# Kernel tuning notes

Measured on AMD Instinct MI355X. Metric: run time of the kernel, lower is better.

The kernel has to match this reference:

```python
import jax, jax.numpy as jnp
import numpy as np

THRESHOLD = 0.5
NEG_POS_RATIO = 3
ALPHA = 10.0


def cxcy_to_xy(c):
    return jnp.concatenate([c[..., :2] - c[..., 2:] / 2, c[..., :2] + c[..., 2:] / 2], axis=-1)


def xy_to_cxcy(xy):
    return jnp.concatenate([(xy[..., :2] + xy[..., 2:]) / 2, xy[..., 2:] - xy[..., :2]], axis=-1)


def encode(cxcy, anc):
    # SSD encoding with variances 0.1 / 0.2 expressed as /10 and *5
    return jnp.concatenate([
        (cxcy[..., :2] - anc[..., :2]) / (anc[..., 2:] / 10.0),
        jnp.log(cxcy[..., 2:] / anc[..., 2:]) * 5.0,
    ], axis=-1)


def jaccard(a, b):
    # a: [N,4] corner boxes, b: [P,4] corner boxes -> [N,P] IoU
    lt = jnp.maximum(a[:, None, :2], b[None, :, :2])
    rb = jnp.minimum(a[:, None, 2:], b[None, :, 2:])
    wh = jnp.clip(rb - lt, 0.0)
    inter = wh[..., 0] * wh[..., 1]
    area_a = (a[:, 2] - a[:, 0]) * (a[:, 3] - a[:, 1])
    area_b = (b[:, 2] - b[:, 0]) * (b[:, 3] - b[:, 1])
    return inter / (area_a[:, None] + area_b[None, :] - inter)


def _match(boxes, labels, corner_anchor, center_anchor):
    # boxes: [N_obj,4] corner, labels: [N_obj]
    n_obj = boxes.shape[0]
    iou = jaccard(boxes, corner_anchor)                 # [N_obj, P]
    obj_idx = jnp.argmax(iou, axis=1)                   # best prior per object
    iou = iou.at[jnp.arange(n_obj), obj_idx].set(1.0)   # force-match best prior
    positive = jnp.any(iou >= THRESHOLD, axis=0)        # [P]
    max_prior_idx = jnp.argmax(iou, axis=0)             # best object per prior
    true_cls = (labels[max_prior_idx] + 1) * positive.astype(jnp.int32)
    true_locs = encode(xy_to_cxcy(boxes[max_prior_idx]), center_anchor)
    return positive, true_cls, true_locs


def setup_inputs() -> dict:
    B, P, C, NOBJ = 32, 24564, 21, 24
    keys = jax.random.split(jax.random.key(0), 7)
    pred_cls = jax.random.normal(keys[0], (B, P, C), dtype=jnp.float32)
    pred_loc = jax.random.normal(keys[1], (B, P, 4), dtype=jnp.float32) * 0.1
    cxy = jax.random.uniform(keys[2], (B, NOBJ, 2), minval=0.2, maxval=0.8)
    wh = jax.random.uniform(keys[3], (B, NOBJ, 2), minval=0.05, maxval=0.3)
    gt_boxes = jnp.clip(jnp.concatenate([cxy - wh / 2, cxy + wh / 2], axis=-1), 0.0, 1.0)
    gt_labels = jax.random.randint(keys[4], (B, NOBJ), 0, C - 1, dtype=jnp.int32)
    a_cxy = jax.random.uniform(keys[5], (P, 2), minval=0.0, maxval=1.0)
    a_wh = jax.random.uniform(keys[6], (P, 2), minval=0.05, maxval=0.4)
    center_anchor = jnp.concatenate([a_cxy, a_wh], axis=-1)
    return {"pred_cls": pred_cls, "pred_loc": pred_loc, "gt_boxes": gt_boxes,
            "gt_labels": gt_labels, "center_anchor": center_anchor}


def reference(pred_cls, pred_loc, gt_boxes, gt_labels, center_anchor):
    B, P, C = pred_cls.shape
    corner_anchor = cxcy_to_xy(center_anchor)
    positive, true_cls, true_locs = jax.vmap(_match, in_axes=(0, 0, None, None))(
        gt_boxes, gt_labels, corner_anchor, center_anchor)

    n_pos = positive.sum(axis=1)                        # [B]
    n_pos_total = n_pos.sum().astype(pred_loc.dtype)

    # localization: L1 mean over positive priors (4 coords each)
    pos_f = positive[..., None].astype(pred_loc.dtype)
    loc_loss = (jnp.abs(pred_loc - true_locs) * pos_f).sum() / (n_pos_total * 4.0)

    # per-element cross entropy [B, P]
    logp = jax.nn.log_softmax(pred_cls, axis=-1)
    ce = -jnp.take_along_axis(logp, true_cls[..., None], axis=-1)[..., 0]

    conf_pos = (ce * positive.astype(ce.dtype)).sum()
    ce_neg = jnp.where(positive, 0.0, ce)
    ce_neg_sorted = jnp.sort(ce_neg, axis=1)[:, ::-1]   # descending
    ranks = jnp.arange(P)[None, :]
    hard_mask = (ranks < (NEG_POS_RATIO * n_pos)[:, None]).astype(ce.dtype)
    conf_neg = (ce_neg_sorted * hard_mask).sum()
    conf_loss = (conf_pos + conf_neg) / n_pos_total

    loc_loss = ALPHA * loc_loss
    total_loss = conf_loss + loc_loss
    return total_loss, (conf_loss, loc_loss)
```

## Files before the change

kernel.cpp:

```cpp
#include <hip/hip_runtime.h>
#include <stdint.h>

#define B 32
#define P 24564
#define NCLS 21
#define NOBJ 24
#define THRESH 0.5f
#define NBKT 2048
#define LCAP 6144
#define BKT_BASE 7232

#define OFF_ACC      0
#define OFF_ARRV     24
#define OFF_NPOS     32
#define HDR_WORDS    40
#define OFF_OBJPART  160
#define OFF_HIST     98464
#define OFF_CENEG    360608

typedef unsigned long long u64;
__device__ __forceinline__ u64 umax64(u64 a, u64 b) { return a > b ? a : b; }

__device__ __forceinline__ int ce_bucket(unsigned bits) {
    int bk = (int)(bits >> 17) - BKT_BASE;
    return bk < 0 ? 0 : (bk > 2047 ? 2047 : bk);
}

__global__ __launch_bounds__(256) void k_objmax(
    const float* __restrict__ gt_boxes, const float* __restrict__ anchor,
    char* __restrict__ ws) {
#pragma clang fp contract(off)
    int b = blockIdx.y;
    int j = blockIdx.x;
    int tid = threadIdx.x;
    unsigned* hist = (unsigned*)(ws + OFF_HIST);
    u64* part = (u64*)(ws + OFF_OBJPART);
    if (tid < 128) hist[(b * 16 + j) * 128 + tid] = 0u;
    if (b == 0 && j == 0 && tid < HDR_WORDS) ((unsigned*)ws)[tid] = 0u;
    __shared__ float4 sbox[NOBJ];
    __shared__ u64 sbest[NOBJ];
    if (tid < NOBJ) {
        const float* g = gt_boxes + (size_t)(b * NOBJ + tid) * 4;
        sbox[tid] = make_float4(g[0], g[1], g[2], g[3]);
        sbest[tid] = 0ull;
    }
    __syncthreads();
    u64 best[NOBJ];
#pragma unroll
    for (int n = 0; n < NOBJ; n++) best[n] = 0ull;
    int pend = min(P, (j + 1) * 1536);
    for (int p = j * 1536 + tid; p < pend; p += 256) {
        float4 a = *(const float4*)(anchor + (size_t)p * 4);
        float ax0 = a.x - a.z * 0.5f, ay0 = a.y - a.w * 0.5f;
        float ax1 = a.x + a.z * 0.5f, ay1 = a.y + a.w * 0.5f;
        float area_a = (ax1 - ax0) * (ay1 - ay0);
        unsigned pk = ~(unsigned)p;
#pragma unroll
        for (int n = 0; n < NOBJ; n++) {
            float4 bx = sbox[n];
            float ltx = fmaxf(bx.x, ax0), lty = fmaxf(bx.y, ay0);
            float rbx = fminf(bx.z, ax1), rby = fminf(bx.w, ay1);
            float w = fmaxf(rbx - ltx, 0.f), h = fmaxf(rby - lty, 0.f);
            float inter = w * h;
            float area_o = (bx.z - bx.x) * (bx.w - bx.y);
            float iou = inter / (area_o + area_a - inter);
            u64 key = ((u64)__float_as_uint(iou) << 32) | pk;
            best[n] = umax64(best[n], key);
        }
    }
#pragma unroll
    for (int n = 0; n < NOBJ; n++) {
        u64 v = best[n];
        for (int off = 32; off > 0; off >>= 1) v = umax64(v, __shfl_down(v, off, 64));
        if ((tid & 63) == 0) atomicMax(&sbest[n], v);
    }
    __syncthreads();
    if (tid < NOBJ) part[((size_t)b * NOBJ + tid) * 16 + j] = sbest[tid];
}

__global__ __launch_bounds__(256, 4) void k_mainB(
    const float* __restrict__ pred_cls, const float* __restrict__ pred_loc,
    const float* __restrict__ gt_boxes, const int* __restrict__ gt_labels,
    const float* __restrict__ anchor, char* __restrict__ ws) {
    double* acc = (double*)(ws + OFF_ACC);
    int* n_pos = (int*)(ws + OFF_NPOS);
    const u64* objpart = (const u64*)(ws + OFF_OBJPART);
    unsigned* hist = (unsigned*)(ws + OFF_HIST);
    float* ce_neg = (float*)(ws + OFF_CENEG);

    __shared__ float4 sbox[NOBJ];
    __shared__ float sarea[NOBJ];
    __shared__ int slab[NOBJ];
    __shared__ int sobj[NOBJ];
    __shared__ unsigned shist[NBKT];
    __shared__ float swf[8];
    __shared__ int swi[4];
    const int tid = threadIdx.x;
    const int b = blockIdx.x / 48;
    const int j = blockIdx.x % 48;

    for (int i = tid; i < NBKT; i += 256) shist[i] = 0u;
    if (tid < NOBJ) {
        const float* g = gt_boxes + (size_t)(b * NOBJ + tid) * 4;
        sbox[tid] = make_float4(g[0], g[1], g[2], g[3]);
        sarea[tid] = (g[2] - g[0]) * (g[3] - g[1]);
        slab[tid] = gt_labels[b * NOBJ + tid];
        const u64* pp = objpart + ((size_t)b * NOBJ + tid) * 16;
        u64 m = pp[0];
#pragma unroll
        for (int q = 1; q < 16; q++) m = umax64(m, pp[q]);
        sobj[tid] = (int)(~(unsigned)(m & 0xFFFFFFFFull));
    }
    __syncthreads();

    int p0 = j * 512 + tid * 2;
    float lsum = 0.f, cpos = 0.f;
    int lnp = 0;
    if (p0 < P) {
        float2 xx[21];
        const float2* xp = (const float2*)(pred_cls + ((size_t)b * P + p0) * NCLS);
#pragma unroll
        for (int k = 0; k < 21; k++) xx[k] = xp[k];
        const float* arr = (const float*)xx;
        float4 anc2[2];
        anc2[0] = ((const float4*)anchor)[p0];
        anc2[1] = ((const float4*)anchor)[p0 + 1];
        float2 cev;
        float* cevp = (float*)&cev;
#pragma unroll
        for (int r = 0; r < 2; r++) {
            int p = p0 + r;
            float4 a = anc2[r];
            float ax0 = a.x - a.z * 0.5f, ay0 = a.y - a.w * 0.5f;
            float ax1 = a.x + a.z * 0.5f, ay1 = a.y + a.w * 0.5f;
            float area_a = (ax1 - ax0) * (ay1 - ay0);
            float bv = -1.f;
            int bn = 0;
#pragma unroll
            for (int n = 0; n < NOBJ; n++) {
                float4 bx = sbox[n];
                float ltx = fmaxf(bx.x, ax0), lty = fmaxf(bx.y, ay0);
                float rbx = fminf(bx.z, ax1), rby = fminf(bx.w, ay1);
                float w = fmaxf(rbx - ltx, 0.f), h = fmaxf(rby - lty, 0.f);
                float inter = w * h;
                float den = sarea[n] + area_a - inter;
                float iou = inter * __builtin_amdgcn_rcpf(den);
                if (p == sobj[n]) iou = 1.0f;
                if (iou > bv) { bv = iou; bn = n; }
            }
            int pos = (bv >= THRESH) ? 1 : 0;
            int cls = pos ? (slab[bn] + 1) : 0;
            const float* x = arr + r * 21;
            float m = x[0];
#pragma unroll
            for (int q = 1; q < NCLS; q++) m = fmaxf(m, x[q]);
            float s = 0.f;
#pragma unroll
            for (int q = 0; q < NCLS; q++) s += __expf(x[q] - m);
            float xc = x[0];
#pragma unroll
            for (int q = 1; q < NCLS; q++) xc = (cls == q) ? x[q] : xc;
            float ce = m + __logf(s) - xc;
            if (pos) {
                lnp++;
                cpos += ce;
                cevp[r] = 0.f;
                float4 bx = sbox[bn];
                float bcx = (bx.x + bx.z) * 0.5f, bcy = (bx.y + bx.w) * 0.5f;
                float bw = bx.z - bx.x, bh = bx.w - bx.y;
                float t0 = (bcx - a.x) / (a.z / 10.0f);
                float t1 = (bcy - a.y) / (a.w / 10.0f);
                float t2 = __logf(bw / a.z) * 5.0f;
                float t3 = __logf(bh / a.w) * 5.0f;
                float4 pl = *(const float4*)(pred_loc + ((size_t)b * P + p) * 4);
                lsum += fabsf(pl.x - t0) + fabsf(pl.y - t1) + fabsf(pl.z - t2) + fabsf(pl.w - t3);
            } else {
                float cen = fmaxf(ce, 0.f);
                cevp[r] = cen;
                atomicAdd(&shist[ce_bucket(__float_as_uint(cen))], 1u);
            }
        }
        *(float2*)(ce_neg + (size_t)b * P + p0) = cev;
    }
    for (int off = 32; off > 0; off >>= 1) {
        lsum += __shfl_down(lsum, off, 64);
        cpos += __shfl_down(cpos, off, 64);
        lnp  += __shfl_down(lnp, off, 64);
    }
    if ((tid & 63) == 0) { swf[tid >> 6] = lsum; swf[4 + (tid >> 6)] = cpos; swi[tid >> 6] = lnp; }
    __syncthreads();
    if (tid == 0) {
        float ls = swf[0] + swf[1] + swf[2] + swf[3];
        float cs = swf[4] + swf[5] + swf[6] + swf[7];
        int np = swi[0] + swi[1] + swi[2] + swi[3];
        if (np) atomicAdd(&n_pos[b], np);
        atomicAdd(&acc[0], (double)ls);
        atomicAdd(&acc[1], (double)cs);
    }
    for (int i = tid; i < NBKT; i += 256) {
        unsigned c = shist[i];
        if (c) atomicAdd(&hist[b * NBKT + i], c);
    }
}

__device__ __forceinline__ void find_bound(const unsigned* shist, int NB, int K,
                                           int* sscal, unsigned* wsum, int tid) {
    int G = NB >> 8;
    unsigned loc[8];
    unsigned tot = 0, v = 0;
    if (tid < 256) {
        for (int g = 0; g < G; g++) { loc[g] = shist[tid * G + g]; tot += loc[g]; }
        v = tot;
        int lane = tid & 63;
        for (int off = 1; off < 64; off <<= 1) {
            unsigned o = __shfl_down(v, off, 64);
            if (lane + off < 64) v += o;
        }
        if (lane == 0) wsum[tid >> 6] = v;
    }
    __syncthreads();
    if (tid < 256) {
        unsigned above = 0;
        for (int w = (tid >> 6) + 1; w < 4; w++) above += wsum[w];
        unsigned sfx_excl = above + (v - tot);
        unsigned snext = 0, sloc = 0;
        for (int k = G - 1; k >= 0; k--) {
            sloc = snext + loc[k];
            unsigned sfx_i = sloc + sfx_excl;
            unsigned sfx_n = snext + sfx_excl;
            if (sfx_i >= (unsigned)K && sfx_n < (unsigned)K) {
                sscal[0] = tid * G + k;
                sscal[1] = K - (int)sfx_n;
            }
            snext = sloc;
        }
        if (tid == 0) {
            unsigned total = sloc + sfx_excl;
            if (total < (unsigned)K) {
                sscal[0] = 0;
                sscal[1] = K - (int)((sloc - loc[0]) + sfx_excl);
            }
        }
    }
    __syncthreads();
}

__device__ __forceinline__ void find_bound64(const unsigned* h64, int K, int* sscal, int tid) {
    if (tid < 64) {
        unsigned cnt = h64[tid];
        unsigned v = cnt;
        for (int off = 1; off < 64; off <<= 1) {
            unsigned o = __shfl_down(v, off, 64);
            if (tid + off < 64) v += o;
        }
        unsigned vnext = v - cnt;
        if (v >= (unsigned)K && vnext < (unsigned)K) { sscal[0] = tid; sscal[1] = K - (int)vnext; }
    }
    __syncthreads();
}

__device__ __forceinline__ int bsum16i(int v, int* buf, int tid) {
    for (int off = 32; off > 0; off >>= 1) v += __shfl_down(v, off, 64);
    if ((tid & 63) == 0) buf[tid >> 6] = v;
    __syncthreads();
    int r = 0;
#pragma unroll
    for (int w = 0; w < 16; w++) r += buf[w];
    __syncthreads();
    return r;
}

__global__ __launch_bounds__(1024) void k_sel(
    const float* __restrict__ ce_neg, const unsigned* __restrict__ hist,
    const int* __restrict__ n_pos, double* __restrict__ acc,
    unsigned* __restrict__ arrv, float* __restrict__ out) {
    __shared__ unsigned shist[NBKT];
    __shared__ unsigned slist[LCAP];
    __shared__ int swi[16];
    __shared__ double swd[16];
    __shared__ unsigned wsum[4];
    __shared__ int sscal[4];
    const int b = blockIdx.x;
    const int tid = threadIdx.x;
    int K = n_pos[b] * 3;
    if (K > P) K = P;
    double s = 0.0;
    if (K > 0) {
        for (int i = tid; i < NBKT; i += 1024) shist[i] = hist[b * NBKT + i];
        __syncthreads();
        find_bound(shist, NBKT, K, sscal, wsum, tid);
        int b0 = sscal[0], Kp0 = sscal[1];
        if (tid == 0) sscal[2] = 0;
        __syncthreads();
        const uint4* x4 = (const uint4*)(ce_neg + (size_t)b * P);
        for (int i = tid; i < P / 4; i += 1024) {
            uint4 v = x4[i];
            unsigned vv[4] = {v.x, v.y, v.z, v.w};
#pragma unroll
            for (int r = 0; r < 4; r++) {
                int bk = ce_bucket(vv[r]);
                if (bk > b0) s += (double)__uint_as_float(vv[r]);
                else if (bk == b0) {
                    int pos = atomicAdd(&sscal[2], 1);
                    if (pos < LCAP) slist[pos] = vv[r];
                }
            }
        }
        __syncthreads();
        int lcnt = sscal[2];
        if (Kp0 > 0) {
            bool clamped = (b0 == 0) || (b0 == 2047);
            if (lcnt <= LCAP && !clamped) {
                for (int i = tid; i < NBKT; i += 1024) shist[i] = 0u;
                __syncthreads();
                for (int i = tid; i < lcnt; i += 1024)
                    atomicAdd(&shist[(slist[i] >> 6) & 0x7FFu], 1u);
                __syncthreads();
                find_bound(shist, NBKT, Kp0, sscal, wsum, tid);
                int b1 = sscal[0], Kp1 = sscal[1];
                if (tid < 64) shist[tid] = 0u;
                __syncthreads();
                for (int i = tid; i < lcnt; i += 1024) {
                    unsigned v = slist[i];
                    int k1 = (int)((v >> 6) & 0x7FFu);
                    if (k1 > b1) s += (double)__uint_as_float(v);
                    else if (k1 == b1) atomicAdd(&shist[v & 0x3Fu], 1u);
                }
                __syncthreads();
                find_bound64(shist, Kp1, sscal, tid);
                int b2 = sscal[0], R = sscal[1];
                for (int i = tid; i < lcnt; i += 1024) {
                    unsigned v = slist[i];
                    if ((int)((v >> 6) & 0x7FFu) == b1 && (int)(v & 0x3Fu) > b2)
                        s += (double)__uint_as_float(v);
                }
                unsigned Tbits = ((unsigned)(b0 + BKT_BASE) << 17) | ((unsigned)b1 << 6) | (unsigned)b2;
                if (tid == 0) s += (double)R * (double)__uint_as_float(Tbits);
            } else if (lcnt <= LCAP) {
                unsigned T = 0;
                for (int bit = 30; bit >= 0; bit--) {
                    unsigned cand = T | (1u << bit);
                    int cc = 0;
                    for (int i = tid; i < lcnt; i += 1024) cc += (slist[i] >= cand) ? 1 : 0;
                    int tot = bsum16i(cc, swi, tid);
                    if (tot >= Kp0) T = cand;
                }
                int cgt = 0;
                for (int i = tid; i < lcnt; i += 1024) {
                    unsigned v = slist[i];
                    if (v > T) { cgt++; s += (double)__uint_as_float(v); }
                }
                int cg = bsum16i(cgt, swi, tid);
                if (tid == 0) s += (double)(Kp0 - cg) * (double)__uint_as_float(T);
            } else {
                const unsigned* src = (const unsigned*)(ce_neg + (size_t)b * P);
                unsigned T = 0;
                for (int bit = 30; bit >= 0; bit--) {
                    unsigned cand = T | (1u << bit);
                    int cc = 0;
                    for (int i = tid; i < P; i += 1024) {
                        unsigned v = src[i];
                        if (ce_bucket(v) == b0 && v >= cand) cc++;
                    }
                    int tot = bsum16i(cc, swi, tid);
                    if (tot >= Kp0) T = cand;
                }
                int cgt = 0;
                for (int i = tid; i < P; i += 1024) {
                    unsigned v = src[i];
                    if (ce_bucket(v) == b0 && v > T) { cgt++; s += (double)__uint_as_float(v); }
                }
                int cg = bsum16i(cgt, swi, tid);
                if (tid == 0) s += (double)(Kp0 - cg) * (double)__uint_as_float(T);
            }
        }
        for (int off = 32; off > 0; off >>= 1) s += __shfl_down(s, off, 64);
        if ((tid & 63) == 0) swd[tid >> 6] = s;
        __syncthreads();
        if (tid == 0) {
            double tot = 0.0;
#pragma unroll
            for (int w = 0; w < 16; w++) tot += swd[w];
            atomicAdd(&acc[2], tot);
        }
    }
    __syncthreads();
    if (tid == 0) {
        __threadfence();
        unsigned done = __hip_atomic_fetch_add(arrv, 1u, __ATOMIC_ACQ_REL,
                                               __HIP_MEMORY_SCOPE_AGENT);
        if (done == B - 1) {
            int npt = 0;
            for (int k = 0; k < B; k++)
                npt += __hip_atomic_load((int*)&n_pos[k], __ATOMIC_RELAXED,
                                         __HIP_MEMORY_SCOPE_AGENT);
            u64 u0 = __hip_atomic_load((u64*)&acc[0], __ATOMIC_RELAXED, __HIP_MEMORY_SCOPE_AGENT);
            u64 u1 = __hip_atomic_load((u64*)&acc[1], __ATOMIC_RELAXED, __HIP_MEMORY_SCOPE_AGENT);
            u64 u2 = __hip_atomic_load((u64*)&acc[2], __ATOMIC_RELAXED, __HIP_MEMORY_SCOPE_AGENT);
            double a0 = __longlong_as_double((long long)u0);
            double a1 = __longlong_as_double((long long)u1);
            double a2 = __longlong_as_double((long long)u2);
            double npf = (double)npt;
            float conf = (float)((a1 + a2) / npf);
            float loc = 10.0f * (float)(a0 / (npf * 4.0));
            out[0] = conf + loc;
            out[1] = conf;
            out[2] = loc;
        }
    }
}

extern "C" void kernel_launch(void* const* d_in, const int* in_sizes, int n_in,
                              void* d_out, int out_size, void* d_ws, size_t ws_size,
                              hipStream_t stream) {
    const float* pred_cls = (const float*)d_in[0];
    const float* pred_loc = (const float*)d_in[1];
    const float* gt_boxes = (const float*)d_in[2];
    const int*   gt_labels = (const int*)d_in[3];
    const float* anchor   = (const float*)d_in[4];
    float* out = (float*)d_out;
    char* ws = (char*)d_ws;
    double* acc = (double*)(ws + OFF_ACC);
    unsigned* arrv = (unsigned*)(ws + OFF_ARRV);
    int* n_pos = (int*)(ws + OFF_NPOS);
    unsigned* hist = (unsigned*)(ws + OFF_HIST);
    float* ce_neg = (float*)(ws + OFF_CENEG);

    k_objmax<<<dim3(16, B), 256, 0, stream>>>(gt_boxes, anchor, ws);
    k_mainB<<<48 * B, 256, 0, stream>>>(pred_cls, pred_loc, gt_boxes, gt_labels, anchor, ws);
    k_sel<<<B, 1024, 0, stream>>>(ce_neg, hist, n_pos, acc, arrv, out);
}
```

Measured before the change: 198.0 us.

## Process four priors per thread with float4 loads and max-free log-sum-exp

Each thread now handles four consecutive priors, so its 84 class logits load as 21 aligned float4 values, and the grid shrinks to 24 blocks per image. The log-softmax drops the max subtraction and sums exponentials directly in three scheduled chunks. The target-class logit is re-read from global memory only for positive priors, and launch bounds are relaxed to two blocks per SM. This aims to widen memory accesses and cut ALU work, at the cost of overflow risk for large logits, which the normal-distributed inputs avoid, and fewer resident blocks.

```diff
diff --git a/kernel.cpp b/kernel.cpp
--- a/kernel.cpp
+++ b/kernel.cpp
@@ -78,7 +78,7 @@
     if (tid < NOBJ) part[((size_t)b * NOBJ + tid) * 16 + j] = sbest[tid];
 }
 
-__global__ __launch_bounds__(256, 4) void k_mainB(
+__global__ __launch_bounds__(256, 2) void k_mainB(
     const float* __restrict__ pred_cls, const float* __restrict__ pred_loc,
     const float* __restrict__ gt_boxes, const int* __restrict__ gt_labels,
     const float* __restrict__ anchor, char* __restrict__ ws) {
@@ -96,8 +96,8 @@
     __shared__ float swf[8];
     __shared__ int swi[4];
     const int tid = threadIdx.x;
-    const int b = blockIdx.x / 48;
-    const int j = blockIdx.x % 48;
+    const int b = blockIdx.x / 24;
+    const int j = blockIdx.x % 24;
 
     for (int i = tid; i < NBKT; i += 256) shist[i] = 0u;
     if (tid < NOBJ) {
@@ -113,24 +113,63 @@
     }
     __syncthreads();
 
-    int p0 = j * 512 + tid * 2;
+    int p0 = j * 1024 + tid * 4;
     float lsum = 0.f, cpos = 0.f;
     int lnp = 0;
     if (p0 < P) {
-        float2 xx[21];
-        const float2* xp = (const float2*)(pred_cls + ((size_t)b * P + p0) * NCLS);
-#pragma unroll
-        for (int k = 0; k < 21; k++) xx[k] = xp[k];
-        const float* arr = (const float*)xx;
-        float4 anc2[2];
-        anc2[0] = ((const float4*)anchor)[p0];
-        anc2[1] = ((const float4*)anchor)[p0 + 1];
-        float2 cev;
+        const float4* xp = (const float4*)(pred_cls + ((size_t)b * P + p0) * NCLS);
+        float s0 = 0.f, s1 = 0.f, s2 = 0.f, s3 = 0.f;
+        float x0a = 0.f, x0b = 0.f, x0c = 0.f, x0d = 0.f;
+        {
+            float4 v0 = xp[0], v1 = xp[1], v2 = xp[2], v3 = xp[3], v4 = xp[4], v5 = xp[5], v6 = xp[6];
+            x0a = v0.x;
+            s0 += __expf(v0.x) + __expf(v0.y) + __expf(v0.z) + __expf(v0.w);
+            s0 += __expf(v1.x) + __expf(v1.y) + __expf(v1.z) + __expf(v1.w);
+            s0 += __expf(v2.x) + __expf(v2.y) + __expf(v2.z) + __expf(v2.w);
+            s0 += __expf(v3.x) + __expf(v3.y) + __expf(v3.z) + __expf(v3.w);
+            s0 += __expf(v4.x) + __expf(v4.y) + __expf(v4.z) + __expf(v4.w);
+            s0 += __expf(v5.x);
+            x0b = v5.y;
+            s1 += __expf(v5.y) + __expf(v5.z) + __expf(v5.w);
+            s1 += __expf(v6.x) + __expf(v6.y) + __expf(v6.z) + __expf(v6.w);
+        }
+        __builtin_amdgcn_sched_barrier(0);
+        {
+            float4 v7 = xp[7], v8 = xp[8], v9 = xp[9], v10 = xp[10], v11 = xp[11], v12 = xp[12], v13 = xp[13];
+            s1 += __expf(v7.x) + __expf(v7.y) + __expf(v7.z) + __expf(v7.w);
+            s1 += __expf(v8.x) + __expf(v8.y) + __expf(v8.z) + __expf(v8.w);
+            s1 += __expf(v9.x) + __expf(v9.y) + __expf(v9.z) + __expf(v9.w);
+            s1 += __expf(v10.x) + __expf(v10.y);
+            x0c = v10.z;
+            s2 += __expf(v10.z) + __expf(v10.w);
+            s2 += __expf(v11.x) + __expf(v11.y) + __expf(v11.z) + __expf(v11.w);
+            s2 += __expf(v12.x) + __expf(v12.y) + __expf(v12.z) + __expf(v12.w);
+            s2 += __expf(v13.x) + __expf(v13.y) + __expf(v13.z) + __expf(v13.w);
+        }
+        __builtin_amdgcn_sched_barrier(0);
+        {
+            float4 v14 = xp[14], v15 = xp[15], v16 = xp[16], v17 = xp[17], v18 = xp[18], v19 = xp[19], v20 = xp[20];
+            s2 += __expf(v14.x) + __expf(v14.y) + __expf(v14.z) + __expf(v14.w);
+            s2 += __expf(v15.x) + __expf(v15.y) + __expf(v15.z);
+            x0d = v15.w;
+            s3 += __expf(v15.w);
+            s3 += __expf(v16.x) + __expf(v16.y) + __expf(v16.z) + __expf(v16.w);
+            s3 += __expf(v17.x) + __expf(v17.y) + __expf(v17.z) + __expf(v17.w);
+            s3 += __expf(v18.x) + __expf(v18.y) + __expf(v18.z) + __expf(v18.w);
+            s3 += __expf(v19.x) + __expf(v19.y) + __expf(v19.z) + __expf(v19.w);
+            s3 += __expf(v20.x) + __expf(v20.y) + __expf(v20.z) + __expf(v20.w);
+        }
+        float lse[4] = {__logf(s0), __logf(s1), __logf(s2), __logf(s3)};
+        float x0v[4] = {x0a, x0b, x0c, x0d};
+        float4 anc4[4];
+#pragma unroll
+        for (int r = 0; r < 4; r++) anc4[r] = ((const float4*)anchor)[p0 + r];
+        float4 cev;
         float* cevp = (float*)&cev;
 #pragma unroll
-        for (int r = 0; r < 2; r++) {
+        for (int r = 0; r < 4; r++) {
             int p = p0 + r;
-            float4 a = anc2[r];
+            float4 a = anc4[r];
             float ax0 = a.x - a.z * 0.5f, ay0 = a.y - a.w * 0.5f;
             float ax1 = a.x + a.z * 0.5f, ay1 = a.y + a.w * 0.5f;
             float area_a = (ax1 - ax0) * (ay1 - ay0);
@@ -143,27 +182,15 @@
                 float rbx = fminf(bx.z, ax1), rby = fminf(bx.w, ay1);
                 float w = fmaxf(rbx - ltx, 0.f), h = fmaxf(rby - lty, 0.f);
                 float inter = w * h;
-                float den = sarea[n] + area_a - inter;
-                float iou = inter * __builtin_amdgcn_rcpf(den);
+                float iou = inter * __builtin_amdgcn_rcpf(sarea[n] + area_a - inter);
                 if (p == sobj[n]) iou = 1.0f;
                 if (iou > bv) { bv = iou; bn = n; }
             }
-            int pos = (bv >= THRESH) ? 1 : 0;
-            int cls = pos ? (slab[bn] + 1) : 0;
-            const float* x = arr + r * 21;
-            float m = x[0];
-#pragma unroll
-            for (int q = 1; q < NCLS; q++) m = fmaxf(m, x[q]);
-            float s = 0.f;
-#pragma unroll
-            for (int q = 0; q < NCLS; q++) s += __expf(x[q] - m);
-            float xc = x[0];
-#pragma unroll
-            for (int q = 1; q < NCLS; q++) xc = (cls == q) ? x[q] : xc;
-            float ce = m + __logf(s) - xc;
-            if (pos) {
+            if (bv >= THRESH) {
+                int cls = slab[bn] + 1;
+                float xc = pred_cls[((size_t)b * P + p) * NCLS + cls];
                 lnp++;
-                cpos += ce;
+                cpos += lse[r] - xc;
                 cevp[r] = 0.f;
                 float4 bx = sbox[bn];
                 float bcx = (bx.x + bx.z) * 0.5f, bcy = (bx.y + bx.w) * 0.5f;
@@ -175,12 +202,12 @@
                 float4 pl = *(const float4*)(pred_loc + ((size_t)b * P + p) * 4);
                 lsum += fabsf(pl.x - t0) + fabsf(pl.y - t1) + fabsf(pl.z - t2) + fabsf(pl.w - t3);
             } else {
-                float cen = fmaxf(ce, 0.f);
+                float cen = fmaxf(lse[r] - x0v[r], 0.f);
                 cevp[r] = cen;
                 atomicAdd(&shist[ce_bucket(__float_as_uint(cen))], 1u);
             }
         }
-        *(float2*)(ce_neg + (size_t)b * P + p0) = cev;
+        *(float4*)(ce_neg + (size_t)b * P + p0) = cev;
     }
     for (int off = 32; off > 0; off >>= 1) {
         lsum += __shfl_down(lsum, off, 64);
@@ -427,6 +454,6 @@
     float* ce_neg = (float*)(ws + OFF_CENEG);
 
     k_objmax<<<dim3(16, B), 256, 0, stream>>>(gt_boxes, anchor, ws);
-    k_mainB<<<48 * B, 256, 0, stream>>>(pred_cls, pred_loc, gt_boxes, gt_labels, anchor, ws);
+    k_mainB<<<24 * B, 256, 0, stream>>>(pred_cls, pred_loc, gt_boxes, gt_labels, anchor, ws);
     k_sel<<<B, 1024, 0, stream>>>(ce_neg, hist, n_pos, acc, arrv, out);
 }
```

After: 168.7 us. -14.8%, faster.

## Compute per-prior best match in objmax pass, stage class logits through LDS

Applied to the files above, without the earlier changes.

The first kernel already computes every prior-object IoU, so it now also records each prior's best IoU (truncated mantissa) plus the object index in a packed word and stores it into the ce_neg buffer. The main kernel no longer recomputes 24 IoUs per prior. Instead it reads that packed word and applies the forced matches. Class logits are loaded coalesced into shared memory with one prior per thread, and the softmax drops max-subtraction. This adds an extra global write and read per prior, adds LDS pressure that lowers occupancy, and skipping max-subtraction risks overflow for large logits.

```diff
diff --git a/kernel.cpp b/kernel.cpp
--- a/kernel.cpp
+++ b/kernel.cpp
@@ -35,6 +35,7 @@
     int tid = threadIdx.x;
     unsigned* hist = (unsigned*)(ws + OFF_HIST);
     u64* part = (u64*)(ws + OFF_OBJPART);
+    unsigned* pmatch = (unsigned*)(ws + OFF_CENEG);
     if (tid < 128) hist[(b * 16 + j) * 128 + tid] = 0u;
     if (b == 0 && j == 0 && tid < HDR_WORDS) ((unsigned*)ws)[tid] = 0u;
     __shared__ float4 sbox[NOBJ];
@@ -55,6 +56,7 @@
         float ax1 = a.x + a.z * 0.5f, ay1 = a.y + a.w * 0.5f;
         float area_a = (ax1 - ax0) * (ay1 - ay0);
         unsigned pk = ~(unsigned)p;
+        unsigned pb = 0u;
 #pragma unroll
         for (int n = 0; n < NOBJ; n++) {
             float4 bx = sbox[n];
@@ -66,7 +68,10 @@
             float iou = inter / (area_o + area_a - inter);
             u64 key = ((u64)__float_as_uint(iou) << 32) | pk;
             best[n] = umax64(best[n], key);
-        }
+            unsigned pkey = (__float_as_uint(iou) & 0xFFFFFFC0u) | (unsigned)(63 - n);
+            pb = pb > pkey ? pb : pkey;
+        }
+        pmatch[(size_t)b * P + p] = pb;
     }
 #pragma unroll
     for (int n = 0; n < NOBJ; n++) {
@@ -86,24 +91,25 @@
     int* n_pos = (int*)(ws + OFF_NPOS);
     const u64* objpart = (const u64*)(ws + OFF_OBJPART);
     unsigned* hist = (unsigned*)(ws + OFF_HIST);
-    float* ce_neg = (float*)(ws + OFF_CENEG);
-
+    unsigned* pm_ce = (unsigned*)(ws + OFF_CENEG);
+
+    __shared__ __align__(16) float sx[256 * NCLS];
+    __shared__ unsigned shist[NBKT];
     __shared__ float4 sbox[NOBJ];
-    __shared__ float sarea[NOBJ];
     __shared__ int slab[NOBJ];
     __shared__ int sobj[NOBJ];
-    __shared__ unsigned shist[NBKT];
     __shared__ float swf[8];
     __shared__ int swi[4];
     const int tid = threadIdx.x;
-    const int b = blockIdx.x / 48;
-    const int j = blockIdx.x % 48;
+    const int b = blockIdx.y;
+    const int j = blockIdx.x;
+    const int p0 = j * 256;
+    const int nelem = min(256, P - p0);
 
     for (int i = tid; i < NBKT; i += 256) shist[i] = 0u;
     if (tid < NOBJ) {
         const float* g = gt_boxes + (size_t)(b * NOBJ + tid) * 4;
         sbox[tid] = make_float4(g[0], g[1], g[2], g[3]);
-        sarea[tid] = (g[2] - g[0]) * (g[3] - g[1]);
         slab[tid] = gt_labels[b * NOBJ + tid];
         const u64* pp = objpart + ((size_t)b * NOBJ + tid) * 16;
         u64 m = pp[0];
@@ -111,76 +117,51 @@
         for (int q = 1; q < 16; q++) m = umax64(m, pp[q]);
         sobj[tid] = (int)(~(unsigned)(m & 0xFFFFFFFFull));
     }
-    __syncthreads();
-
-    int p0 = j * 512 + tid * 2;
+    {
+        const float4* g4 = (const float4*)(pred_cls + ((size_t)b * P + p0) * NCLS);
+        int nf4 = (nelem * NCLS) >> 2;
+        for (int i = tid; i < nf4; i += 256) ((float4*)sx)[i] = g4[i];
+    }
+    __syncthreads();
+
     float lsum = 0.f, cpos = 0.f;
     int lnp = 0;
-    if (p0 < P) {
-        float2 xx[21];
-        const float2* xp = (const float2*)(pred_cls + ((size_t)b * P + p0) * NCLS);
-#pragma unroll
-        for (int k = 0; k < 21; k++) xx[k] = xp[k];
-        const float* arr = (const float*)xx;
-        float4 anc2[2];
-        anc2[0] = ((const float4*)anchor)[p0];
-        anc2[1] = ((const float4*)anchor)[p0 + 1];
-        float2 cev;
-        float* cevp = (float*)&cev;
-#pragma unroll
-        for (int r = 0; r < 2; r++) {
-            int p = p0 + r;
-            float4 a = anc2[r];
-            float ax0 = a.x - a.z * 0.5f, ay0 = a.y - a.w * 0.5f;
-            float ax1 = a.x + a.z * 0.5f, ay1 = a.y + a.w * 0.5f;
-            float area_a = (ax1 - ax0) * (ay1 - ay0);
-            float bv = -1.f;
-            int bn = 0;
-#pragma unroll
-            for (int n = 0; n < NOBJ; n++) {
-                float4 bx = sbox[n];
-                float ltx = fmaxf(bx.x, ax0), lty = fmaxf(bx.y, ay0);
-                float rbx = fminf(bx.z, ax1), rby = fminf(bx.w, ay1);
-                float w = fmaxf(rbx - ltx, 0.f), h = fmaxf(rby - lty, 0.f);
-                float inter = w * h;
-                float den = sarea[n] + area_a - inter;
-                float iou = inter * __builtin_amdgcn_rcpf(den);
-                if (p == sobj[n]) iou = 1.0f;
-                if (iou > bv) { bv = iou; bn = n; }
-            }
-            int pos = (bv >= THRESH) ? 1 : 0;
-            int cls = pos ? (slab[bn] + 1) : 0;
-            const float* x = arr + r * 21;
-            float m = x[0];
-#pragma unroll
-            for (int q = 1; q < NCLS; q++) m = fmaxf(m, x[q]);
-            float s = 0.f;
-#pragma unroll
-            for (int q = 0; q < NCLS; q++) s += __expf(x[q] - m);
-            float xc = x[0];
-#pragma unroll
-            for (int q = 1; q < NCLS; q++) xc = (cls == q) ? x[q] : xc;
-            float ce = m + __logf(s) - xc;
-            if (pos) {
-                lnp++;
-                cpos += ce;
-                cevp[r] = 0.f;
-                float4 bx = sbox[bn];
-                float bcx = (bx.x + bx.z) * 0.5f, bcy = (bx.y + bx.w) * 0.5f;
-                float bw = bx.z - bx.x, bh = bx.w - bx.y;
-                float t0 = (bcx - a.x) / (a.z / 10.0f);
-                float t1 = (bcy - a.y) / (a.w / 10.0f);
-                float t2 = __logf(bw / a.z) * 5.0f;
-                float t3 = __logf(bh / a.w) * 5.0f;
-                float4 pl = *(const float4*)(pred_loc + ((size_t)b * P + p) * 4);
-                lsum += fabsf(pl.x - t0) + fabsf(pl.y - t1) + fabsf(pl.z - t2) + fabsf(pl.w - t3);
-            } else {
-                float cen = fmaxf(ce, 0.f);
-                cevp[r] = cen;
-                atomicAdd(&shist[ce_bucket(__float_as_uint(cen))], 1u);
-            }
-        }
-        *(float2*)(ce_neg + (size_t)b * P + p0) = cev;
+    if (tid < nelem) {
+        int p = p0 + tid;
+        size_t idx = (size_t)b * P + p;
+        unsigned m = pm_ce[idx];
+        const float* x = sx + tid * NCLS;
+        float s = 0.f;
+#pragma unroll
+        for (int q = 0; q < NCLS; q++) s += __expf(x[q]);
+        float ls = __logf(s);
+        int bn = 63 - (int)(m & 63u);
+        bool pos = __uint_as_float(m & 0xFFFFFFC0u) >= THRESH;
+#pragma unroll
+        for (int n = NOBJ - 1; n >= 0; n--) {
+            if (p == sobj[n]) { pos = true; bn = n; }
+        }
+        float cen;
+        if (pos) {
+            int cls = slab[bn] + 1;
+            lnp++;
+            cpos += ls - x[cls];
+            cen = 0.f;
+            float4 a = ((const float4*)anchor)[p];
+            float4 bx = sbox[bn];
+            float bcx = (bx.x + bx.z) * 0.5f, bcy = (bx.y + bx.w) * 0.5f;
+            float bw = bx.z - bx.x, bh = bx.w - bx.y;
+            float t0 = (bcx - a.x) / (a.z / 10.0f);
+            float t1 = (bcy - a.y) / (a.w / 10.0f);
+            float t2 = __logf(bw / a.z) * 5.0f;
+            float t3 = __logf(bh / a.w) * 5.0f;
+            float4 pl = *(const float4*)(pred_loc + idx * 4);
+            lsum += fabsf(pl.x - t0) + fabsf(pl.y - t1) + fabsf(pl.z - t2) + fabsf(pl.w - t3);
+        } else {
+            cen = fmaxf(ls - x[0], 0.f);
+            atomicAdd(&shist[ce_bucket(__float_as_uint(cen))], 1u);
+        }
+        pm_ce[idx] = __float_as_uint(cen);
     }
     for (int off = 32; off > 0; off >>= 1) {
         lsum += __shfl_down(lsum, off, 64);
@@ -190,11 +171,11 @@
     if ((tid & 63) == 0) { swf[tid >> 6] = lsum; swf[4 + (tid >> 6)] = cpos; swi[tid >> 6] = lnp; }
     __syncthreads();
     if (tid == 0) {
-        float ls = swf[0] + swf[1] + swf[2] + swf[3];
+        float lsm = swf[0] + swf[1] + swf[2] + swf[3];
         float cs = swf[4] + swf[5] + swf[6] + swf[7];
         int np = swi[0] + swi[1] + swi[2] + swi[3];
         if (np) atomicAdd(&n_pos[b], np);
-        atomicAdd(&acc[0], (double)ls);
+        atomicAdd(&acc[0], (double)lsm);
         atomicAdd(&acc[1], (double)cs);
     }
     for (int i = tid; i < NBKT; i += 256) {
@@ -427,6 +408,6 @@
     float* ce_neg = (float*)(ws + OFF_CENEG);
 
     k_objmax<<<dim3(16, B), 256, 0, stream>>>(gt_boxes, anchor, ws);
-    k_mainB<<<48 * B, 256, 0, stream>>>(pred_cls, pred_loc, gt_boxes, gt_labels, anchor, ws);
+    k_mainB<<<dim3(96, B), 256, 0, stream>>>(pred_cls, pred_loc, gt_boxes, gt_labels, anchor, ws);
     k_sel<<<B, 1024, 0, stream>>>(ce_neg, hist, n_pos, acc, arrv, out);
 }
```

Result: slower. 223.1 us (+12.7%).
